# Kernel tuning notes

Measured on AMD Instinct MI355X. Metric: run time of the kernel, lower is better.

Reference implementation:

```python
import jax, jax.numpy as jnp
import numpy as np

H = 8   # heads
C = 64  # per-head channels (gnn_hidden_dim)
HID = H * C  # 512
IN_CH = 6
EMB = 64
U, M = 16, 512
N_NODES = U * M  # 8192
N_EDGES = 131072


def _tconv(x, src, dst, Wq, bq, Wk, bk, Wv, bv, Ws, bs):
    """PyG TransformerConv (concat=True, root_weight=True, beta=False, eval mode)."""
    N = x.shape[0]
    q = (x @ Wq + bq).reshape(N, H, C)
    k = (x @ Wk + bk).reshape(N, H, C)
    v = (x @ Wv + bv).reshape(N, H, C)
    # per-edge attention scores: query at dst (target i), key at src (source j)
    score = jnp.einsum('ehc,ehc->eh', q[dst], k[src]) / jnp.sqrt(jnp.float32(C))
    # segment softmax over incoming edges of each dst node
    mx = jax.ops.segment_max(score, dst, num_segments=N)
    ex = jnp.exp(score - mx[dst])
    denom = jax.ops.segment_sum(ex, dst, num_segments=N)
    alpha = ex / (denom[dst] + 1e-16)  # [E, H]
    msg = alpha[..., None] * v[src]    # [E, H, C]
    out = jax.ops.segment_sum(msg, dst, num_segments=N).reshape(N, HID)
    return out + x @ Ws + bs  # root/skip connection


def setup_inputs() -> dict:
    key = jax.random.key(0)
    ks = iter(jax.random.split(key, 64))
    s = 0.05

    def lin(k, i, o):
        k1, k2 = jax.random.split(k)
        return (jax.random.normal(k1, (i, o), jnp.float32) * s,
                jax.random.normal(k2, (o,), jnp.float32) * s)

    inp = {}
    inp['mission_coords'] = jax.random.uniform(next(ks), (M, 2), jnp.float32)
    inp['uavs_info'] = jax.random.uniform(next(ks), (U, 2), jnp.float32)
    inp['speeds'] = jax.random.uniform(next(ks), (U,), jnp.float32)
    inp['dist_matrix'] = jax.random.uniform(next(ks), (U, M), jnp.float32)
    inp['timetogo_matrix'] = jax.random.uniform(next(ks), (U, M), jnp.float32)
    inp['action_mask'] = jax.random.randint(next(ks), (U, M), 0, 2, jnp.int32)
    inp['edge_index'] = jax.random.randint(next(ks), (2, N_EDGES), 0, N_NODES, jnp.int64)
    inp['batch'] = jnp.zeros((U,), jnp.int64)

    # layer 0 (in=6)
    inp['Wq0'], inp['bq0'] = lin(next(ks), IN_CH, HID)
    inp['Wk0'], inp['bk0'] = lin(next(ks), IN_CH, HID)
    inp['Wv0'], inp['bv0'] = lin(next(ks), IN_CH, HID)
    inp['Ws0'], inp['bs0'] = lin(next(ks), IN_CH, HID)
    # layers 1..3 stacked (in=512)
    for nm in ['Wq', 'Wk', 'Wv', 'Ws']:
        Ws_, bs_ = [], []
        for _ in range(3):
            w, b = lin(next(ks), HID, HID)
            Ws_.append(w); bs_.append(b)
        inp[nm] = jnp.stack(Ws_)
        inp['b' + nm[1:].lower()] = jnp.stack(bs_)
    inp['Wout'], inp['bout'] = lin(next(ks), HID, EMB)
    inp['Wa1'], inp['ba1'] = lin(next(ks), EMB + 3, 128)
    inp['Wa2'], inp['ba2'] = lin(next(ks), 128, 1)
    inp['Wc1'], inp['bc1'] = lin(next(ks), EMB + 3, 128)
    inp['Wc2'], inp['bc2'] = lin(next(ks), 128, 1)
    return inp


def reference(mission_coords, uavs_info, speeds, dist_matrix, timetogo_matrix,
              action_mask, edge_index, batch,
              Wq0, bq0, Wk0, bk0, Wv0, bv0, Ws0, bs0,
              Wq, bq, Wk, bk, Wv, bv, Ws, bs,
              Wout, bout, Wa1, ba1, Wa2, ba2, Wc1, bc1, Wc2, bc2):
    u, m = uavs_info.shape[0], mission_coords.shape[0]
    mc = jnp.broadcast_to(mission_coords[None], (u, m, 2))
    mask_e = action_mask[..., None].astype(jnp.float32)
    sp_e = jnp.broadcast_to(speeds[:, None, None], (u, m, 1))
    x = jnp.concatenate([mc, mask_e, sp_e, dist_matrix[..., None],
                         timetogo_matrix[..., None]], axis=-1).reshape(u * m, IN_CH)
    src, dst = edge_index[0], edge_index[1]
    x = jax.nn.relu(_tconv(x, src, dst, Wq0, bq0, Wk0, bk0, Wv0, bv0, Ws0, bs0))
    for l in range(3):
        x = jax.nn.relu(_tconv(x, src, dst, Wq[l], bq[l], Wk[l], bk[l],
                               Wv[l], bv[l], Ws[l], bs[l]))
    x = x @ Wout + bout  # [U*M, EMB]
    uav_emb = x.reshape(u, m, EMB).sum(axis=1)  # sum pooling over missions
    combined = jnp.concatenate([uavs_info, uav_emb, speeds[:, None]], axis=-1)
    logits = jax.nn.relu(combined @ Wa1 + ba1) @ Wa2 + ba2  # [U, 1]
    action_probs = jax.nn.softmax(logits, axis=-1)
    state_values = (jax.nn.relu(combined @ Wc1 + bc1) @ Wc2 + bc2).squeeze()
    return action_probs, state_values
```

## Files before the change

### kernel.cpp

```cpp
#include <hip/hip_runtime.h>
#include <hip/hip_bf16.h>
#include <math.h>

#define NNODES 8192
#define NEDGES 131072
#define HID    512
#define UU     16
#define MM     512
#define NQKVS  2048
#define KVREC  1536

#if __has_builtin(__builtin_amdgcn_cvt_pk_f32_fp8) && __has_builtin(__builtin_amdgcn_cvt_pk_fp8_f32)
#define HAVE_FP8 1
#else
#define HAVE_FP8 0
#endif

#define KSCALE 16.0f
#define KISCALE (0.125f / 16.0f)

typedef __attribute__((ext_vector_type(8))) short bf16x8;
typedef __attribute__((ext_vector_type(4))) float f32x4;
typedef __attribute__((ext_vector_type(2))) float f32x2;

__device__ __forceinline__ float bf2f(ushort u) {
    return __uint_as_float(((unsigned)u) << 16);
}
__device__ __forceinline__ ushort f2bf(float f) {
    unsigned x = __float_as_uint(f);
    return (ushort)((x + 0x7fffu + ((x >> 16) & 1u)) >> 16);
}

__global__ __launch_bounds__(256) void k_wtb(
    const float* __restrict__ Wq, const float* __restrict__ Wk,
    const float* __restrict__ Wv, const float* __restrict__ Ws,
    const float* __restrict__ bq, const float* __restrict__ bk,
    const float* __restrict__ bv, const float* __restrict__ bs,
    ushort* __restrict__ Wt, float* __restrict__ bcat, int* __restrict__ zbuf)
{
    __shared__ float tile[64][65];
    int z = blockIdx.z;
    int t = threadIdx.x;
    if (z == 12) {
        int id = blockIdx.y * 8 + blockIdx.x;
        if (id < 24) {
            int i = id * 256 + t;
            int l = i >> 11, j = i & 2047;
            int which = j >> 9, jj = j & 511;
            const float* b = which == 0 ? bq : which == 1 ? bk : which == 2 ? bv : bs;
            bcat[i] = b[l * HID + jj];
        } else if (id < 56) {
            int idx = (id - 24) * 512 + t * 2;
            zbuf[idx] = 0; zbuf[idx + 1] = 0;
        }
        return;
    }
    int l = z >> 2, which = z & 3;
    const float* src = (which == 0 ? Wq : which == 1 ? Wk : which == 2 ? Wv : Ws)
                       + (size_t)l * HID * HID;
    int k0 = blockIdx.x * 64, c0 = blockIdx.y * 64;
#pragma unroll
    for (int i = 0; i < 16; ++i) {
        int idx = i * 256 + t;
        int r = idx >> 6, c = idx & 63;
        tile[r][c] = src[(size_t)(k0 + r) * HID + c0 + c];
    }
    __syncthreads();
    ushort* dst = Wt + ((size_t)l * NQKVS + which * HID + c0) * HID + k0;
#pragma unroll
    for (int i = 0; i < 16; ++i) {
        int idx = i * 256 + t;
        int r = idx >> 6, c = idx & 63;
        dst[(size_t)r * HID + c] = f2bf(tile[c][r]);
    }
}

__global__ __launch_bounds__(256) void k_lin0(
    const float* __restrict__ mc, const float* __restrict__ speeds,
    const float* __restrict__ dist, const float* __restrict__ ttg,
    const int* __restrict__ mask,
    const float* __restrict__ Wq0, const float* __restrict__ bq0,
    const float* __restrict__ Wk0, const float* __restrict__ bk0,
    const float* __restrict__ Wv0, const float* __restrict__ bv0,
    const float* __restrict__ Ws0, const float* __restrict__ bs0,
    ushort* __restrict__ Y, unsigned char* __restrict__ KV)
{
    int n = blockIdx.x;
    int u = n >> 9, m = n & 511;
    float x[6];
    x[0] = mc[m * 2 + 0];
    x[1] = mc[m * 2 + 1];
    x[2] = (float)mask[u * MM + m];
    x[3] = speeds[u];
    x[4] = dist[u * MM + m];
    x[5] = ttg[u * MM + m];

    int j = threadIdx.x;
    int col0 = j * 8;
    int which = col0 >> 9, jj = col0 & 511;
    const float* W = which == 0 ? Wq0 : which == 1 ? Wk0 : which == 2 ? Wv0 : Ws0;
    const float* b = which == 0 ? bq0 : which == 1 ? bk0 : which == 2 ? bv0 : bs0;
    float s[8];
#pragma unroll
    for (int uu = 0; uu < 8; ++uu) s[uu] = b[jj + uu];
#pragma unroll
    for (int t = 0; t < 6; ++t)
#pragma unroll
        for (int uu = 0; uu < 8; ++uu)
            s[uu] = fmaf(x[t], W[t * HID + jj + uu], s[uu]);
    if (which == 0 || which == 3) {
        bf16x8 o8;
#pragma unroll
        for (int uu = 0; uu < 8; ++uu) o8[uu] = (short)f2bf(s[uu]);
        *(bf16x8*)(Y + (size_t)n * NQKVS + col0) = o8;
    } else if (which == 2) {
        bf16x8 o8;
#pragma unroll
        for (int uu = 0; uu < 8; ++uu) o8[uu] = (short)f2bf(s[uu]);
        *(bf16x8*)(KV + (size_t)n * KVREC + 512 + jj * 2) = o8;
    } else {
#if HAVE_FP8
        int w0 = __builtin_amdgcn_cvt_pk_fp8_f32(s[0] * KSCALE, s[1] * KSCALE, 0, false);
        w0     = __builtin_amdgcn_cvt_pk_fp8_f32(s[2] * KSCALE, s[3] * KSCALE, w0, true);
        int w1 = __builtin_amdgcn_cvt_pk_fp8_f32(s[4] * KSCALE, s[5] * KSCALE, 0, false);
        w1     = __builtin_amdgcn_cvt_pk_fp8_f32(s[6] * KSCALE, s[7] * KSCALE, w1, true);
        uint2 uu2; uu2.x = (unsigned)w0; uu2.y = (unsigned)w1;
        *(uint2*)(KV + (size_t)n * KVREC + jj) = uu2;
#else
        bf16x8 o8;
#pragma unroll
        for (int uu = 0; uu < 8; ++uu) o8[uu] = (short)f2bf(s[uu]);
        *(bf16x8*)(KV + (size_t)n * KVREC + jj * 2) = o8;
#endif
    }
}

#define GBM 128
#define GBN 128
#define GBK 64
#define TILEB (GBM * GBK * 2)
#define BUFB  (2 * TILEB)

__device__ __forceinline__ void stage_tile(
    const ushort* __restrict__ Ag, const ushort* __restrict__ Bg,
    char* __restrict__ base, int t)
{
    const int lane = t & 63;
    const int w = t >> 6;
    const int r8 = lane >> 3;
    const int c  = lane & 7;
    const int csw = c ^ r8;
#pragma unroll
    for (int i = 0; i < 4; ++i) {
        int r0 = (w * 4 + i) * 8;
        __builtin_amdgcn_global_load_lds(
            (const __attribute__((address_space(1))) void*)(Ag + (size_t)(r0 + r8) * HID + csw * 8),
            (__attribute__((address_space(3))) void*)(base + r0 * 128 + lane * 16), 16, 0, 0);
        __builtin_amdgcn_global_load_lds(
            (const __attribute__((address_space(1))) void*)(Bg + (size_t)(r0 + r8) * HID + csw * 8),
            (__attribute__((address_space(3))) void*)(base + TILEB + r0 * 128 + lane * 16), 16, 0, 0);
    }
}

__global__ __launch_bounds__(256, 2) void k_gemm(
    const ushort* __restrict__ A,
    const ushort* __restrict__ Bt,
    const float* __restrict__ bias,
    ushort* __restrict__ Y,
    unsigned char* __restrict__ KV)
{
    __shared__ char lds[2 * BUFB];
    const int t = threadIdx.x;
    const int bid = blockIdx.x;
    const int xcd = bid & 7;
    const int ii  = bid >> 3;
    const int mi  = (xcd << 3) | (ii & 7);
    const int ni  = ii >> 3;
    const int m0 = mi * GBM, n0 = ni * GBN;

    const int wid = t >> 6, lane = t & 63;
    const int wr = wid >> 1, wc = wid & 1;
    const int l15 = lane & 15, lkq = lane >> 4;

    f32x4 acc[4][4] = {};

    const ushort* Ab = A + (size_t)m0 * HID;
    const ushort* Bb = Bt + (size_t)n0 * HID;

    stage_tile(Ab, Bb, lds, t);
    int cur = 0;
    const int NKS = HID / GBK;
    for (int T = 0; T < NKS; ++T) {
        __syncthreads();
        if (T + 1 < NKS)
            stage_tile(Ab + (T + 1) * GBK, Bb + (T + 1) * GBK,
                       lds + (cur ^ 1) * BUFB, t);
        const char* la = lds + cur * BUFB;
        const char* lb = la + TILEB;
#pragma unroll
        for (int kh = 0; kh < 2; ++kh) {
            const int kq = kh * 4 + lkq;
            const int sw = (kq ^ (l15 & 7)) << 4;
            bf16x8 a[4], b[4];
#pragma unroll
            for (int i = 0; i < 4; ++i)
                a[i] = *(const bf16x8*)(la + (wr * 64 + i * 16 + l15) * 128 + sw);
#pragma unroll
            for (int j = 0; j < 4; ++j)
                b[j] = *(const bf16x8*)(lb + (wc * 64 + j * 16 + l15) * 128 + sw);
#pragma unroll
            for (int i = 0; i < 4; ++i)
#pragma unroll
                for (int j = 0; j < 4; ++j)
                    acc[i][j] = __builtin_amdgcn_mfma_f32_16x16x32_bf16(a[i], b[j], acc[i][j], 0, 0, 0);
        }
        cur ^= 1;
    }

    const int whichq = n0 >> 9;
#pragma unroll
    for (int i = 0; i < 4; ++i) {
        int row = m0 + wr * 64 + i * 16 + lkq * 4;
#pragma unroll
        for (int j = 0; j < 4; ++j) {
            int col = n0 + wc * 64 + j * 16 + l15;
            float bc = bias[col];
            f32x4 r = acc[i][j];
#pragma unroll
            for (int g = 0; g < 4; ++g) {
                float val = r[g] + bc;
                if (whichq == 0 || whichq == 3) {
                    Y[(size_t)(row + g) * NQKVS + col] = f2bf(val);
                } else if (whichq == 2) {
                    *(ushort*)(KV + (size_t)(row + g) * KVREC + 512 + (col - 1024) * 2) = f2bf(val);
                } else {
#if HAVE_FP8
                    int pk = __builtin_amdgcn_cvt_pk_fp8_f32(val * KSCALE, val * KSCALE, 0, false);
                    KV[(size_t)(row + g) * KVREC + (col - 512)] = (unsigned char)(pk & 0xff);
#else
                    *(ushort*)(KV + (size_t)(row + g) * KVREC + (col - 512) * 2) = f2bf(val);
#endif
                }
            }
        }
    }
}

__global__ __launch_bounds__(256) void k_hist(const int* __restrict__ dst, int* __restrict__ cnt)
{
    int e = blockIdx.x * blockDim.x + threadIdx.x;
    if (e < NEDGES) atomicAdd(&cnt[dst[e]], 1);
}

__global__ __launch_bounds__(1024) void k_scan(const int* __restrict__ cnt, int* __restrict__ indptr)
{
    __shared__ int wsum[16];
    __shared__ int woff[16];
    int t = threadIdx.x;
    int base = t * 8;
    int v[8];
    int s = 0;
#pragma unroll
    for (int i = 0; i < 8; ++i) { v[i] = cnt[base + i]; s += v[i]; }
    int lane = t & 63, w = t >> 6;
    int incl = s;
#pragma unroll
    for (int off = 1; off < 64; off <<= 1) {
        int u = __shfl_up(incl, off);
        if (lane >= off) incl += u;
    }
    if (lane == 63) wsum[w] = incl;
    __syncthreads();
    if (t == 0) {
        int run = 0;
#pragma unroll
        for (int i = 0; i < 16; ++i) { woff[i] = run; run += wsum[i]; }
    }
    __syncthreads();
    int run = woff[w] + incl - s;
#pragma unroll
    for (int i = 0; i < 8; ++i) { indptr[base + i] = run; run += v[i]; }
    if (t == 1023) indptr[NNODES] = run;
}

__global__ __launch_bounds__(256) void k_scatter(
    const int* __restrict__ src, const int* __restrict__ dst,
    const int* __restrict__ indptr, int* __restrict__ cursor, int* __restrict__ ssrc)
{
    int e = blockIdx.x * blockDim.x + threadIdx.x;
    if (e >= NEDGES) return;
    int d = dst[e];
    int p = atomicAdd(&cursor[d], 1);
    ssrc[indptr[d] + p] = src[e];
}

__global__ __launch_bounds__(256) void k_attn(
    const int* __restrict__ indptr, const int* __restrict__ ssrc,
    const ushort* __restrict__ Y,
    const unsigned char* __restrict__ KV,
    ushort* __restrict__ X)
{
    int n = blockIdx.x * 4 + (threadIdx.x >> 6);
    if (n >= NNODES) return;
    int l = threadIdx.x & 63;
    int cbase = l * 8;
    const ushort* yq = Y + (size_t)n * NQKVS + cbase;
    float qf[8];
    {
        bf16x8 q8 = *(const bf16x8*)yq;
#pragma unroll
        for (int j = 0; j < 8; ++j) qf[j] = bf2f((ushort)q8[j]);
    }
    float mrun = -INFINITY, ssum = 0.f;
    float acc[8] = {};
    int e0 = indptr[n], e1 = indptr[n + 1];
#if HAVE_FP8
    uint2 ka = {}, kb = {};
#define KLOAD(K_, base_) K_ = *(const uint2*)((base_) + cbase)
#else
    bf16x8 ka = {}, kb = {};
#define KLOAD(K_, base_) K_ = *(const bf16x8*)((base_) + cbase * 2)
#endif
    bf16x8 va = {}, vb = {};
    if (e0 < e1) {
        const unsigned char* r = KV + (size_t)ssrc[e0] * KVREC;
        KLOAD(ka, r);
        va = *(const bf16x8*)(r + 512 + cbase * 2);
    }
    if (e0 + 1 < e1) {
        const unsigned char* r = KV + (size_t)ssrc[e0 + 1] * KVREC;
        KLOAD(kb, r);
        vb = *(const bf16x8*)(r + 512 + cbase * 2);
    }
    for (int e = e0; e < e1; ++e) {
        auto k8 = ka; bf16x8 v8 = va;
        ka = kb; va = vb;
        int en = e + 2;
        if (en < e1) {
            const unsigned char* r = KV + (size_t)ssrc[en] * KVREC;
            KLOAD(kb, r);
            vb = *(const bf16x8*)(r + 512 + cbase * 2);
        }
        float part = 0.f;
#if HAVE_FP8
        {
            f32x2 k01 = __builtin_amdgcn_cvt_pk_f32_fp8((int)k8.x, false);
            f32x2 k23 = __builtin_amdgcn_cvt_pk_f32_fp8((int)k8.x, true);
            f32x2 k45 = __builtin_amdgcn_cvt_pk_f32_fp8((int)k8.y, false);
            f32x2 k67 = __builtin_amdgcn_cvt_pk_f32_fp8((int)k8.y, true);
            part = fmaf(qf[0], k01.x, part); part = fmaf(qf[1], k01.y, part);
            part = fmaf(qf[2], k23.x, part); part = fmaf(qf[3], k23.y, part);
            part = fmaf(qf[4], k45.x, part); part = fmaf(qf[5], k45.y, part);
            part = fmaf(qf[6], k67.x, part); part = fmaf(qf[7], k67.y, part);
        }
        const float smul = KISCALE;
#else
#pragma unroll
        for (int j = 0; j < 8; ++j) part = fmaf(qf[j], bf2f((ushort)k8[j]), part);
        const float smul = 0.125f;
#endif
        part += __shfl_xor(part, 1);
        part += __shfl_xor(part, 2);
        part += __shfl_xor(part, 4);
        float score = part * smul;
        float mnew = fmaxf(mrun, score);
        float sc = __expf(mrun - mnew);
        float p = __expf(score - mnew);
        ssum = ssum * sc + p;
#pragma unroll
        for (int j = 0; j < 8; ++j)
            acc[j] = fmaf(acc[j], sc, p * bf2f((ushort)v8[j]));
        mrun = mnew;
    }
    float inv = ssum > 0.f ? 1.f / ssum : 0.f;
    bf16x8 o8;
#pragma unroll
    for (int j = 0; j < 8; ++j) {
        float o = fmaxf(fmaf(acc[j], inv, bf2f(yq[1536 + j])), 0.f);
        o8[j] = (short)f2bf(o);
    }
    *(bf16x8*)(X + (size_t)n * HID + cbase) = o8;
}

__global__ __launch_bounds__(512) void k_pool(const ushort* __restrict__ X, float* __restrict__ xsumP)
{
    int u = blockIdx.x;
    int pp = blockIdx.y;
    int c = threadIdx.x;
    const ushort* base = X + ((size_t)u * MM + pp * 64) * HID + c;
    float s = 0.f;
    for (int m = 0; m < 64; ++m) s += bf2f(base[(size_t)m * HID]);
    xsumP[((size_t)u * 8 + pp) * HID + c] = s;
}

__global__ __launch_bounds__(512) void k_embhead(
    const float* __restrict__ xsumP, const float* __restrict__ Wout,
    const float* __restrict__ bout,
    const float* __restrict__ uavs, const float* __restrict__ speeds,
    const float* __restrict__ Wc1, const float* __restrict__ bc1,
    const float* __restrict__ Wc2, const float* __restrict__ bc2,
    float* __restrict__ out)
{
    __shared__ float xs[HID];
    __shared__ float comb[67];
    __shared__ float red[128];
    int u = blockIdx.x, c = threadIdx.x;
    float s = 0.f;
#pragma unroll
    for (int p = 0; p < 8; ++p) s += xsumP[((size_t)u * 8 + p) * HID + c];
    xs[c] = s;
    __syncthreads();
    if (c < 64) {
        float a = 0.f;
        for (int i = 0; i < HID; ++i) a = fmaf(xs[i], Wout[i * 64 + c], a);
        comb[2 + c] = a + 512.0f * bout[c];
    }
    if (c == 64) { comb[0] = uavs[u * 2]; comb[1] = uavs[u * 2 + 1]; }
    if (c == 65) comb[66] = speeds[u];
    __syncthreads();
    if (c < 128) {
        float a = bc1[c];
        for (int i = 0; i < 67; ++i) a = fmaf(comb[i], Wc1[i * 128 + c], a);
        a = fmaxf(a, 0.f);
        red[c] = a * Wc2[c];
    }
    __syncthreads();
    for (int sft = 64; sft > 0; sft >>= 1) {
        if (c < sft) red[c] += red[c + sft];
        __syncthreads();
    }
    if (c == 0) {
        out[u]      = 1.0f;
        out[16 + u] = red[0] + bc2[0];
    }
}

extern "C" void kernel_launch(void* const* d_in, const int* in_sizes, int n_in,
                              void* d_out, int out_size, void* d_ws, size_t ws_size,
                              hipStream_t stream)
{
    const float* mission_coords = (const float*)d_in[0];
    const float* uavs_info      = (const float*)d_in[1];
    const float* speeds         = (const float*)d_in[2];
    const float* dist_matrix    = (const float*)d_in[3];
    const float* timetogo       = (const float*)d_in[4];
    const int*   action_mask    = (const int*)d_in[5];
    const int*   edge_index     = (const int*)d_in[6];
    const float* Wq0 = (const float*)d_in[8];  const float* bq0 = (const float*)d_in[9];
    const float* Wk0 = (const float*)d_in[10]; const float* bk0 = (const float*)d_in[11];
    const float* Wv0 = (const float*)d_in[12]; const float* bv0 = (const float*)d_in[13];
    const float* Ws0 = (const float*)d_in[14]; const float* bs0 = (const float*)d_in[15];
    const float* Wq  = (const float*)d_in[16]; const float* bq  = (const float*)d_in[17];
    const float* Wk  = (const float*)d_in[18]; const float* bk  = (const float*)d_in[19];
    const float* Wv  = (const float*)d_in[20]; const float* bv  = (const float*)d_in[21];
    const float* Ws  = (const float*)d_in[22]; const float* bs  = (const float*)d_in[23];
    const float* Wout = (const float*)d_in[24]; const float* bout = (const float*)d_in[25];
    const float* Wc1 = (const float*)d_in[30]; const float* bc1 = (const float*)d_in[31];
    const float* Wc2 = (const float*)d_in[32]; const float* bc2 = (const float*)d_in[33];
    float* out = (float*)d_out;

    const int* e_src = edge_index;
    const int* e_dst = edge_index + NEDGES;

    char* p = (char*)d_ws;
    ushort* Ybf = (ushort*)p;  p += (size_t)NNODES * NQKVS * 2;
    ushort* Xbf = (ushort*)p;  p += (size_t)NNODES * HID * 2;
    ushort* Wt  = (ushort*)p;  p += (size_t)3 * NQKVS * HID * 2;
    unsigned char* KV = (unsigned char*)p; p += (size_t)NNODES * KVREC;
    float* bcat = (float*)p;   p += (size_t)3 * NQKVS * 4;
    float* xsumP = (float*)p;  p += (size_t)UU * 8 * HID * 4;
    int* cnt    = (int*)p;     p += (size_t)NNODES * 4;
    int* cursor = (int*)p;     p += (size_t)NNODES * 4;
    int* indptr = (int*)p;     p += (size_t)(NNODES + 1) * 4;
    int* ssrc   = (int*)p;     p += (size_t)NEDGES * 4;

    k_wtb<<<dim3(8, 8, 13), 256, 0, stream>>>(Wq, Wk, Wv, Ws, bq, bk, bv, bs,
                                              Wt, bcat, cnt);
    k_hist<<<NEDGES / 256, 256, 0, stream>>>(e_dst, cnt);
    k_scan<<<1, 1024, 0, stream>>>(cnt, indptr);
    k_scatter<<<NEDGES / 256, 256, 0, stream>>>(e_src, e_dst, indptr, cursor, ssrc);

    k_lin0<<<NNODES, 256, 0, stream>>>(mission_coords, speeds, dist_matrix, timetogo,
                                       action_mask, Wq0, bq0, Wk0, bk0, Wv0, bv0,
                                       Ws0, bs0, Ybf, KV);
    k_attn<<<NNODES / 4, 256, 0, stream>>>(indptr, ssrc, Ybf, KV, Xbf);

    const int ngblocks = (NNODES / GBM) * (NQKVS / GBN);
    for (int l = 0; l < 3; ++l) {
        k_gemm<<<ngblocks, 256, 0, stream>>>(Xbf, Wt + (size_t)l * NQKVS * HID,
                                             bcat + l * NQKVS, Ybf, KV);
        k_attn<<<NNODES / 4, 256, 0, stream>>>(indptr, ssrc, Ybf, KV, Xbf);
    }

    k_pool<<<dim3(UU, 8), 512, 0, stream>>>(Xbf, xsumP);
    k_embhead<<<UU, 512, 0, stream>>>(xsumP, Wout, bout, uavs_info, speeds,
                                      Wc1, bc1, Wc2, bc2, out);
}
```

Before: 268.8 us.

## Fuse hist+scan, scatter+lin0, pooling into attention; compact Q/skip buffer

Merges histogram and prefix scan into one kernel using a last-block-done counter, and folds the CSR scatter into the layer-0 linear kernel as extra blocks. Removes the separate pooling kernel by having the final attention layer write per-4-node partial sums that the head kernel reduces. Shrinks the Y buffer to hold only Q and skip columns. Aims to cut launch count and memory traffic, at the cost of a serial single-block scan and a larger partial-sum reduction in the head.

Result: slower. 305.3 us (+13.6%).

```diff
diff --git a/kernel.cpp b/kernel.cpp
--- a/kernel.cpp
+++ b/kernel.cpp
@@ -7,13 +7,16 @@
 #define HID    512
 #define UU     16
 #define MM     512
-#define NQKVS  2048
-#define KVREC  1536
+#define NQS    1024
 
 #if __has_builtin(__builtin_amdgcn_cvt_pk_f32_fp8) && __has_builtin(__builtin_amdgcn_cvt_pk_fp8_f32)
 #define HAVE_FP8 1
+#define KVREC  1536
+#define KOFF_V 512
 #else
 #define HAVE_FP8 0
+#define KVREC  2048
+#define KOFF_V 1024
 #endif
 
 #define KSCALE 16.0f
@@ -49,9 +52,9 @@
             int which = j >> 9, jj = j & 511;
             const float* b = which == 0 ? bq : which == 1 ? bk : which == 2 ? bv : bs;
             bcat[i] = b[l * HID + jj];
-        } else if (id < 56) {
-            int idx = (id - 24) * 512 + t * 2;
-            zbuf[idx] = 0; zbuf[idx + 1] = 0;
+        } else if (id <= 56) {
+            zbuf[(id - 24) * 512 + t * 2] = 0;
+            zbuf[(id - 24) * 512 + t * 2 + 1] = 0;
         }
         return;
     }
@@ -66,7 +69,7 @@
         tile[r][c] = src[(size_t)(k0 + r) * HID + c0 + c];
     }
     __syncthreads();
-    ushort* dst = Wt + ((size_t)l * NQKVS + which * HID + c0) * HID + k0;
+    ushort* dst = Wt + ((size_t)l * 2048 + which * HID + c0) * HID + k0;
 #pragma unroll
     for (int i = 0; i < 16; ++i) {
         int idx = i * 256 + t;
@@ -75,7 +78,39 @@
     }
 }
 
-__global__ __launch_bounds__(256) void k_lin0(
+__global__ __launch_bounds__(256) void k_histscan(
+    const int* __restrict__ dst, int* __restrict__ cnt,
+    int* __restrict__ indptr, int* __restrict__ done)
+{
+    int e = blockIdx.x * 256 + threadIdx.x;
+    atomicAdd(&cnt[dst[e]], 1);
+    __threadfence();
+    __shared__ int amlast;
+    if (threadIdx.x == 0)
+        amlast = (atomicAdd(done, 1) == (int)gridDim.x - 1);
+    __syncthreads();
+    if (!amlast) return;
+    __shared__ int sums[256];
+    __shared__ int offs[256];
+    int t = threadIdx.x;
+    int base = t * 32;
+    int s = 0;
+    for (int i = 0; i < 32; ++i) s += cnt[base + i];
+    sums[t] = s;
+    __syncthreads();
+    if (t == 0) {
+        int run = 0;
+        for (int i = 0; i < 256; ++i) { offs[i] = run; run += sums[i]; }
+    }
+    __syncthreads();
+    int off = offs[t];
+    for (int i = 0; i < 32; ++i) { indptr[base + i] = off; off += cnt[base + i]; }
+    if (t == 255) indptr[NNODES] = off;
+}
+
+__global__ __launch_bounds__(256) void k_scatlin0(
+    const int* __restrict__ src, const int* __restrict__ dst,
+    const int* __restrict__ indptr, int* __restrict__ cursor, int* __restrict__ ssrc,
     const float* __restrict__ mc, const float* __restrict__ speeds,
     const float* __restrict__ dist, const float* __restrict__ ttg,
     const int* __restrict__ mask,
@@ -85,7 +120,14 @@
     const float* __restrict__ Ws0, const float* __restrict__ bs0,
     ushort* __restrict__ Y, unsigned char* __restrict__ KV)
 {
-    int n = blockIdx.x;
+    if (blockIdx.x < 512) {
+        int e = blockIdx.x * 256 + threadIdx.x;
+        int d = dst[e];
+        int p = atomicAdd(&cursor[d], 1);
+        ssrc[indptr[d] + p] = src[e];
+        return;
+    }
+    int n = blockIdx.x - 512;
     int u = n >> 9, m = n & 511;
     float x[6];
     x[0] = mc[m * 2 + 0];
@@ -112,12 +154,12 @@
         bf16x8 o8;
 #pragma unroll
         for (int uu = 0; uu < 8; ++uu) o8[uu] = (short)f2bf(s[uu]);
-        *(bf16x8*)(Y + (size_t)n * NQKVS + col0) = o8;
+        *(bf16x8*)(Y + (size_t)n * NQS + (which == 0 ? jj : 512 + jj)) = o8;
     } else if (which == 2) {
         bf16x8 o8;
 #pragma unroll
         for (int uu = 0; uu < 8; ++uu) o8[uu] = (short)f2bf(s[uu]);
-        *(bf16x8*)(KV + (size_t)n * KVREC + 512 + jj * 2) = o8;
+        *(bf16x8*)(KV + (size_t)n * KVREC + KOFF_V + jj * 2) = o8;
     } else {
 #if HAVE_FP8
         int w0 = __builtin_amdgcn_cvt_pk_fp8_f32(s[0] * KSCALE, s[1] * KSCALE, 0, false);
@@ -229,10 +271,12 @@
 #pragma unroll
             for (int g = 0; g < 4; ++g) {
                 float val = r[g] + bc;
-                if (whichq == 0 || whichq == 3) {
-                    Y[(size_t)(row + g) * NQKVS + col] = f2bf(val);
+                if (whichq == 0) {
+                    Y[(size_t)(row + g) * NQS + col] = f2bf(val);
+                } else if (whichq == 3) {
+                    Y[(size_t)(row + g) * NQS + (col - 1024)] = f2bf(val);
                 } else if (whichq == 2) {
-                    *(ushort*)(KV + (size_t)(row + g) * KVREC + 512 + (col - 1024) * 2) = f2bf(val);
+                    *(ushort*)(KV + (size_t)(row + g) * KVREC + KOFF_V + (col - 1024) * 2) = f2bf(val);
                 } else {
 #if HAVE_FP8
                     int pk = __builtin_amdgcn_cvt_pk_fp8_f32(val * KSCALE, val * KSCALE, 0, false);
@@ -246,65 +290,20 @@
     }
 }
 
-__global__ __launch_bounds__(256) void k_hist(const int* __restrict__ dst, int* __restrict__ cnt)
-{
-    int e = blockIdx.x * blockDim.x + threadIdx.x;
-    if (e < NEDGES) atomicAdd(&cnt[dst[e]], 1);
-}
-
-__global__ __launch_bounds__(1024) void k_scan(const int* __restrict__ cnt, int* __restrict__ indptr)
-{
-    __shared__ int wsum[16];
-    __shared__ int woff[16];
-    int t = threadIdx.x;
-    int base = t * 8;
-    int v[8];
-    int s = 0;
-#pragma unroll
-    for (int i = 0; i < 8; ++i) { v[i] = cnt[base + i]; s += v[i]; }
-    int lane = t & 63, w = t >> 6;
-    int incl = s;
-#pragma unroll
-    for (int off = 1; off < 64; off <<= 1) {
-        int u = __shfl_up(incl, off);
-        if (lane >= off) incl += u;
-    }
-    if (lane == 63) wsum[w] = incl;
-    __syncthreads();
-    if (t == 0) {
-        int run = 0;
-#pragma unroll
-        for (int i = 0; i < 16; ++i) { woff[i] = run; run += wsum[i]; }
-    }
-    __syncthreads();
-    int run = woff[w] + incl - s;
-#pragma unroll
-    for (int i = 0; i < 8; ++i) { indptr[base + i] = run; run += v[i]; }
-    if (t == 1023) indptr[NNODES] = run;
-}
-
-__global__ __launch_bounds__(256) void k_scatter(
-    const int* __restrict__ src, const int* __restrict__ dst,
-    const int* __restrict__ indptr, int* __restrict__ cursor, int* __restrict__ ssrc)
-{
-    int e = blockIdx.x * blockDim.x + threadIdx.x;
-    if (e >= NEDGES) return;
-    int d = dst[e];
-    int p = atomicAdd(&cursor[d], 1);
-    ssrc[indptr[d] + p] = src[e];
-}
-
 __global__ __launch_bounds__(256) void k_attn(
     const int* __restrict__ indptr, const int* __restrict__ ssrc,
     const ushort* __restrict__ Y,
     const unsigned char* __restrict__ KV,
-    ushort* __restrict__ X)
-{
+    ushort* __restrict__ X,
+    float* __restrict__ xsumP128,
+    int last)
+{
+    __shared__ float pbuf[4][512];
     int n = blockIdx.x * 4 + (threadIdx.x >> 6);
-    if (n >= NNODES) return;
+    int wv = threadIdx.x >> 6;
     int l = threadIdx.x & 63;
     int cbase = l * 8;
-    const ushort* yq = Y + (size_t)n * NQKVS + cbase;
+    const ushort* yq = Y + (size_t)n * NQS + cbase;
     float qf[8];
     {
         bf16x8 q8 = *(const bf16x8*)yq;
@@ -325,12 +324,12 @@
     if (e0 < e1) {
         const unsigned char* r = KV + (size_t)ssrc[e0] * KVREC;
         KLOAD(ka, r);
-        va = *(const bf16x8*)(r + 512 + cbase * 2);
+        va = *(const bf16x8*)(r + KOFF_V + cbase * 2);
     }
     if (e0 + 1 < e1) {
         const unsigned char* r = KV + (size_t)ssrc[e0 + 1] * KVREC;
         KLOAD(kb, r);
-        vb = *(const bf16x8*)(r + 512 + cbase * 2);
+        vb = *(const bf16x8*)(r + KOFF_V + cbase * 2);
     }
     for (int e = e0; e < e1; ++e) {
         auto k8 = ka; bf16x8 v8 = va;
@@ -339,7 +338,7 @@
         if (en < e1) {
             const unsigned char* r = KV + (size_t)ssrc[en] * KVREC;
             KLOAD(kb, r);
-            vb = *(const bf16x8*)(r + 512 + cbase * 2);
+            vb = *(const bf16x8*)(r + KOFF_V + cbase * 2);
         }
         float part = 0.f;
 #if HAVE_FP8
@@ -373,28 +372,33 @@
         mrun = mnew;
     }
     float inv = ssum > 0.f ? 1.f / ssum : 0.f;
-    bf16x8 o8;
-#pragma unroll
-    for (int j = 0; j < 8; ++j) {
-        float o = fmaxf(fmaf(acc[j], inv, bf2f(yq[1536 + j])), 0.f);
-        o8[j] = (short)f2bf(o);
-    }
-    *(bf16x8*)(X + (size_t)n * HID + cbase) = o8;
-}
-
-__global__ __launch_bounds__(512) void k_pool(const ushort* __restrict__ X, float* __restrict__ xsumP)
-{
-    int u = blockIdx.x;
-    int pp = blockIdx.y;
-    int c = threadIdx.x;
-    const ushort* base = X + ((size_t)u * MM + pp * 64) * HID + c;
-    float s = 0.f;
-    for (int m = 0; m < 64; ++m) s += bf2f(base[(size_t)m * HID]);
-    xsumP[((size_t)u * 8 + pp) * HID + c] = s;
+    float o[8];
+#pragma unroll
+    for (int j = 0; j < 8; ++j)
+        o[j] = fmaxf(fmaf(acc[j], inv, bf2f(yq[512 + j])), 0.f);
+
+    if (!last) {
+        bf16x8 o8;
+#pragma unroll
+        for (int j = 0; j < 8; ++j) o8[j] = (short)f2bf(o[j]);
+        *(bf16x8*)(X + (size_t)n * HID + cbase) = o8;
+        return;
+    }
+#pragma unroll
+    for (int j = 0; j < 8; ++j) pbuf[wv][cbase + j] = o[j];
+    __syncthreads();
+    int n0 = blockIdx.x * 4;
+    int u = n0 >> 9, pblk = (n0 & 511) >> 2;
+    float* dstp = xsumP128 + ((size_t)u * 128 + pblk) * 512;
+#pragma unroll
+    for (int rep = 0; rep < 2; ++rep) {
+        int c = rep * 256 + threadIdx.x;
+        dstp[c] = pbuf[0][c] + pbuf[1][c] + pbuf[2][c] + pbuf[3][c];
+    }
 }
 
 __global__ __launch_bounds__(512) void k_embhead(
-    const float* __restrict__ xsumP, const float* __restrict__ Wout,
+    const float* __restrict__ xsumP128, const float* __restrict__ Wout,
     const float* __restrict__ bout,
     const float* __restrict__ uavs, const float* __restrict__ speeds,
     const float* __restrict__ Wc1, const float* __restrict__ bc1,
@@ -405,9 +409,9 @@
     __shared__ float comb[67];
     __shared__ float red[128];
     int u = blockIdx.x, c = threadIdx.x;
+    const float* base = xsumP128 + (size_t)u * 128 * 512 + c;
     float s = 0.f;
-#pragma unroll
-    for (int p = 0; p < 8; ++p) s += xsumP[((size_t)u * 8 + p) * HID + c];
+    for (int p = 0; p < 128; ++p) s += base[p * 512];
     xs[c] = s;
     __syncthreads();
     if (c < 64) {
@@ -463,36 +467,36 @@
     const int* e_dst = edge_index + NEDGES;
 
     char* p = (char*)d_ws;
-    ushort* Ybf = (ushort*)p;  p += (size_t)NNODES * NQKVS * 2;
+    ushort* Ybf = (ushort*)p;  p += (size_t)NNODES * NQS * 2;
     ushort* Xbf = (ushort*)p;  p += (size_t)NNODES * HID * 2;
-    ushort* Wt  = (ushort*)p;  p += (size_t)3 * NQKVS * HID * 2;
+    ushort* Wt  = (ushort*)p;  p += (size_t)3 * 2048 * HID * 2;
     unsigned char* KV = (unsigned char*)p; p += (size_t)NNODES * KVREC;
-    float* bcat = (float*)p;   p += (size_t)3 * NQKVS * 4;
-    float* xsumP = (float*)p;  p += (size_t)UU * 8 * HID * 4;
+    float* bcat = (float*)p;   p += (size_t)3 * 2048 * 4;
+    float* xsumP128 = (float*)p; p += (size_t)UU * 128 * HID * 4;
     int* cnt    = (int*)p;     p += (size_t)NNODES * 4;
     int* cursor = (int*)p;     p += (size_t)NNODES * 4;
+    int* done   = (int*)p;     p += (size_t)512 * 4;
     int* indptr = (int*)p;     p += (size_t)(NNODES + 1) * 4;
     int* ssrc   = (int*)p;     p += (size_t)NEDGES * 4;
 
     k_wtb<<<dim3(8, 8, 13), 256, 0, stream>>>(Wq, Wk, Wv, Ws, bq, bk, bv, bs,
                                               Wt, bcat, cnt);
-    k_hist<<<NEDGES / 256, 256, 0, stream>>>(e_dst, cnt);
-    k_scan<<<1, 1024, 0, stream>>>(cnt, indptr);
-    k_scatter<<<NEDGES / 256, 256, 0, stream>>>(e_src, e_dst, indptr, cursor, ssrc);
-
-    k_lin0<<<NNODES, 256, 0, stream>>>(mission_coords, speeds, dist_matrix, timetogo,
-                                       action_mask, Wq0, bq0, Wk0, bk0, Wv0, bv0,
-                                       Ws0, bs0, Ybf, KV);
-    k_attn<<<NNODES / 4, 256, 0, stream>>>(indptr, ssrc, Ybf, KV, Xbf);
-
-    const int ngblocks = (NNODES / GBM) * (NQKVS / GBN);
+    k_histscan<<<NEDGES / 256, 256, 0, stream>>>(e_dst, cnt, indptr, done);
+
+    k_scatlin0<<<512 + NNODES, 256, 0, stream>>>(
+        e_src, e_dst, indptr, cursor, ssrc,
+        mission_coords, speeds, dist_matrix, timetogo, action_mask,
+        Wq0, bq0, Wk0, bk0, Wv0, bv0, Ws0, bs0, Ybf, KV);
+    k_attn<<<NNODES / 4, 256, 0, stream>>>(indptr, ssrc, Ybf, KV, Xbf, xsumP128, 0);
+
+    const int ngblocks = (NNODES / GBM) * (2048 / GBN);
     for (int l = 0; l < 3; ++l) {
-        k_gemm<<<ngblocks, 256, 0, stream>>>(Xbf, Wt + (size_t)l * NQKVS * HID,
-                                             bcat + l * NQKVS, Ybf, KV);
-        k_attn<<<NNODES / 4, 256, 0, stream>>>(indptr, ssrc, Ybf, KV, Xbf);
-    }
-
-    k_pool<<<dim3(UU, 8), 512, 0, stream>>>(Xbf, xsumP);
-    k_embhead<<<UU, 512, 0, stream>>>(xsumP, Wout, bout, uavs_info, speeds,
+        k_gemm<<<ngblocks, 256, 0, stream>>>(Xbf, Wt + (size_t)l * 2048 * HID,
+                                             bcat + l * 2048, Ybf, KV);
+        k_attn<<<NNODES / 4, 256, 0, stream>>>(indptr, ssrc, Ybf, KV, Xbf,
+                                               xsumP128, l == 2 ? 1 : 0);
+    }
+
+    k_embhead<<<UU, 512, 0, stream>>>(xsumP128, Wout, bout, uavs_info, speeds,
                                       Wc1, bc1, Wc2, bc2, out);
 }
```

## Restructure QKVS GEMM into 256x128 tiles with triple-buffered LDS pipeline

Applied to the files above, without the earlier changes.

The GEMM block tile grows from 128x128 to 256x128 and runs with 512 threads (8 waves). The LDS double buffer becomes a triple buffer in dynamic shared memory, loads are issued two tiles ahead, and explicit vmcnt waits and raw s_barrier calls replace __syncthreads. s_setprio is raised around the MFMA bursts. The aim is to hide global-to-LDS latency and cut B-tile reloads, at the cost of 144KB LDS per block, one block per CU, and fragile hand-written waitcnt logic.

Measured after the change: 272.8 us. Within noise of the previous version (+1.5%).

```diff
diff --git a/kernel.cpp b/kernel.cpp
--- a/kernel.cpp
+++ b/kernel.cpp
@@ -135,47 +135,51 @@
     }
 }
 
-#define GBM 128
+#define GBM 256
 #define GBN 128
 #define GBK 64
-#define TILEB (GBM * GBK * 2)
-#define BUFB  (2 * TILEB)
-
-__device__ __forceinline__ void stage_tile(
+#define ATILE 32768
+#define BTILE 16384
+#define SLOTB (ATILE + BTILE)
+#define NTILES 8
+
+#define VMCNT(n) asm volatile("s_waitcnt vmcnt(" #n ")" ::: "memory")
+
+__device__ __forceinline__ void stage_unit(
     const ushort* __restrict__ Ag, const ushort* __restrict__ Bg,
-    char* __restrict__ base, int t)
-{
-    const int lane = t & 63;
-    const int w = t >> 6;
-    const int r8 = lane >> 3;
-    const int c  = lane & 7;
-    const int csw = c ^ r8;
-#pragma unroll
-    for (int i = 0; i < 4; ++i) {
-        int r0 = (w * 4 + i) * 8;
+    char* __restrict__ buf, int t, int u)
+{
+    int slot = u * 512 + t;
+    if (slot < 2048) {
+        int row = slot >> 3, c = slot & 7;
+        int csw = c ^ (row & 7);
         __builtin_amdgcn_global_load_lds(
-            (const __attribute__((address_space(1))) void*)(Ag + (size_t)(r0 + r8) * HID + csw * 8),
-            (__attribute__((address_space(3))) void*)(base + r0 * 128 + lane * 16), 16, 0, 0);
+            (const __attribute__((address_space(1))) void*)(Ag + (size_t)row * HID + csw * 8),
+            (__attribute__((address_space(3))) void*)(buf + slot * 16), 16, 0, 0);
+    } else {
+        int s2 = slot - 2048;
+        int row = s2 >> 3, c = s2 & 7;
+        int csw = c ^ (row & 7);
         __builtin_amdgcn_global_load_lds(
-            (const __attribute__((address_space(1))) void*)(Bg + (size_t)(r0 + r8) * HID + csw * 8),
-            (__attribute__((address_space(3))) void*)(base + TILEB + r0 * 128 + lane * 16), 16, 0, 0);
-    }
-}
-
-__global__ __launch_bounds__(256, 2) void k_gemm(
+            (const __attribute__((address_space(1))) void*)(Bg + (size_t)row * HID + csw * 8),
+            (__attribute__((address_space(3))) void*)(buf + ATILE + s2 * 16), 16, 0, 0);
+    }
+}
+
+__global__ __launch_bounds__(512, 1) void k_gemm(
     const ushort* __restrict__ A,
     const ushort* __restrict__ Bt,
     const float* __restrict__ bias,
     ushort* __restrict__ Y,
     unsigned char* __restrict__ KV)
 {
-    __shared__ char lds[2 * BUFB];
+    extern __shared__ char lds[];
     const int t = threadIdx.x;
     const int bid = blockIdx.x;
     const int xcd = bid & 7;
     const int ii  = bid >> 3;
-    const int mi  = (xcd << 3) | (ii & 7);
-    const int ni  = ii >> 3;
+    const int mi  = (xcd << 2) | (ii & 3);
+    const int ni  = ii >> 2;
     const int m0 = mi * GBM, n0 = ni * GBN;
 
     const int wid = t >> 6, lane = t & 63;
@@ -187,43 +191,69 @@
     const ushort* Ab = A + (size_t)m0 * HID;
     const ushort* Bb = Bt + (size_t)n0 * HID;
 
-    stage_tile(Ab, Bb, lds, t);
-    int cur = 0;
-    const int NKS = HID / GBK;
-    for (int T = 0; T < NKS; ++T) {
-        __syncthreads();
-        if (T + 1 < NKS)
-            stage_tile(Ab + (T + 1) * GBK, Bb + (T + 1) * GBK,
-                       lds + (cur ^ 1) * BUFB, t);
-        const char* la = lds + cur * BUFB;
-        const char* lb = la + TILEB;
-#pragma unroll
-        for (int kh = 0; kh < 2; ++kh) {
-            const int kq = kh * 4 + lkq;
-            const int sw = (kq ^ (l15 & 7)) << 4;
+#pragma unroll
+    for (int u = 0; u < 6; ++u) stage_unit(Ab, Bb, lds, t, u);
+#pragma unroll
+    for (int u = 0; u < 6; ++u) stage_unit(Ab + GBK, Bb + GBK, lds + SLOTB, t, u);
+    VMCNT(6);
+    __builtin_amdgcn_s_barrier();
+    __builtin_amdgcn_sched_barrier(0);
+
+    const int arow = wr * 64;
+    const int brow = wc * 64;
+#pragma unroll
+    for (int T = 0; T < NTILES; ++T) {
+        char* cbuf = lds + (T % 3) * SLOTB;
+        char* sbuf = lds + ((T + 2) % 3) * SLOTB;
+        const ushort* An = Ab + (T + 2) * GBK;
+        const ushort* Bn = Bb + (T + 2) * GBK;
+#pragma unroll
+        for (int ph = 0; ph < 2; ++ph) {
+            if (T + 2 < NTILES) {
+                stage_unit(An, Bn, sbuf, t, ph * 3 + 0);
+                stage_unit(An, Bn, sbuf, t, ph * 3 + 1);
+                stage_unit(An, Bn, sbuf, t, ph * 3 + 2);
+            }
+            __builtin_amdgcn_sched_barrier(0);
             bf16x8 a[4], b[4];
 #pragma unroll
-            for (int i = 0; i < 4; ++i)
-                a[i] = *(const bf16x8*)(la + (wr * 64 + i * 16 + l15) * 128 + sw);
-#pragma unroll
-            for (int j = 0; j < 4; ++j)
-                b[j] = *(const bf16x8*)(lb + (wc * 64 + j * 16 + l15) * 128 + sw);
+            for (int i = 0; i < 4; ++i) {
+                int row = arow + i * 16 + l15;
+                int kq = ph * 4 + lkq;
+                a[i] = *(const bf16x8*)(cbuf + row * 128 + ((kq ^ (row & 7)) << 4));
+            }
+#pragma unroll
+            for (int j = 0; j < 4; ++j) {
+                int row = brow + j * 16 + l15;
+                int kq = ph * 4 + lkq;
+                b[j] = *(const bf16x8*)(cbuf + ATILE + row * 128 + ((kq ^ (row & 7)) << 4));
+            }
+            __builtin_amdgcn_s_setprio(1);
 #pragma unroll
             for (int i = 0; i < 4; ++i)
 #pragma unroll
                 for (int j = 0; j < 4; ++j)
                     acc[i][j] = __builtin_amdgcn_mfma_f32_16x16x32_bf16(a[i], b[j], acc[i][j], 0, 0, 0);
+            __builtin_amdgcn_s_setprio(0);
+            __builtin_amdgcn_sched_barrier(0);
+            if (ph == 0) {
+                __builtin_amdgcn_s_barrier();
+                __builtin_amdgcn_sched_barrier(0);
+            }
         }
-        cur ^= 1;
+        if (T < NTILES - 2) { VMCNT(6); }
+        else if (T == NTILES - 2) { VMCNT(0); }
+        __builtin_amdgcn_s_barrier();
+        __builtin_amdgcn_sched_barrier(0);
     }
 
     const int whichq = n0 >> 9;
 #pragma unroll
     for (int i = 0; i < 4; ++i) {
-        int row = m0 + wr * 64 + i * 16 + lkq * 4;
+        int row = m0 + arow + i * 16 + lkq * 4;
 #pragma unroll
         for (int j = 0; j < 4; ++j) {
-            int col = n0 + wc * 64 + j * 16 + l15;
+            int col = n0 + brow + j * 16 + l15;
             float bc = bias[col];
             f32x4 r = acc[i][j];
 #pragma unroll
@@ -474,6 +504,13 @@
     int* indptr = (int*)p;     p += (size_t)(NNODES + 1) * 4;
     int* ssrc   = (int*)p;     p += (size_t)NEDGES * 4;
 
+    static bool attr_done = false;
+    if (!attr_done) {
+        hipFuncSetAttribute((const void*)k_gemm,
+                            hipFuncAttributeMaxDynamicSharedMemorySize, 3 * SLOTB);
+        attr_done = true;
+    }
+
     k_wtb<<<dim3(8, 8, 13), 256, 0, stream>>>(Wq, Wk, Wv, Ws, bq, bk, bv, bs,
                                               Wt, bcat, cnt);
     k_hist<<<NEDGES / 256, 256, 0, stream>>>(e_dst, cnt);
@@ -487,8 +524,8 @@
 
     const int ngblocks = (NNODES / GBM) * (NQKVS / GBN);
     for (int l = 0; l < 3; ++l) {
-        k_gemm<<<ngblocks, 256, 0, stream>>>(Xbf, Wt + (size_t)l * NQKVS * HID,
-                                             bcat + l * NQKVS, Ybf, KV);
+        k_gemm<<<ngblocks, 512, 3 * SLOTB, stream>>>(Xbf, Wt + (size_t)l * NQKVS * HID,
+                                                     bcat + l * NQKVS, Ybf, KV);
         k_attn<<<NNODES / 4, 256, 0, stream>>>(indptr, ssrc, Ybf, KV, Xbf);
     }
 
```
